# Optimization experiments

Hardware: AMD Instinct MI355X
Metric: run time of the kernel (lower is better)

The kernel has to match this reference:

```python
import jax, jax.numpy as jnp
import numpy as np

B, S, D = 4, 2048, 1024
NUM_HEADS = 16
KQ = D // NUM_HEADS  # 64


def setup_inputs() -> dict:
    key = jax.random.key(0)
    ks = jax.random.split(key, 4)
    # he_uniform fan_in = D: limit = sqrt(6/fan_in)
    lim = np.sqrt(6.0 / D).astype(np.float32)
    x = jax.random.normal(ks[0], (B, S, D), dtype=jnp.float32)
    Wq = jax.random.uniform(ks[1], (D, KQ), minval=-lim, maxval=lim, dtype=jnp.float32)
    Wk = jax.random.uniform(ks[2], (D, KQ), minval=-lim, maxval=lim, dtype=jnp.float32)
    Wv = jax.random.uniform(ks[3], (D, KQ), minval=-lim, maxval=lim, dtype=jnp.float32)
    Bq = jnp.zeros((S, KQ), dtype=jnp.float32)
    Bk = jnp.zeros((S, KQ), dtype=jnp.float32)
    Bv = jnp.zeros((S, KQ), dtype=jnp.float32)
    return {"x": x, "Wq": Wq, "Bq": Bq, "Wk": Wk, "Bk": Bk, "Wv": Wv, "Bv": Bv}


def reference(x, Wq, Bq, Wk, Bk, Wv, Bv):
    # Q/K/V: [B,S,KQ]; biases are per-position [S,KQ], broadcast over batch
    Q = jnp.einsum('bsd,dk->bsk', x, Wq) + Bq
    K = jnp.einsum('bsd,dk->bsk', x, Wk) + Bk
    V = jnp.einsum('bsd,dk->bsk', x, Wv) + Bv
    scale = 1.0 / jnp.sqrt(jnp.float32(KQ))
    scores = jnp.einsum('bqk,bsk->bqs', Q, K) * scale  # [B,S,S]
    attn = jax.nn.softmax(scores, axis=-1)
    return jnp.einsum('bqs,bsk->bqk', attn, V)  # [B,S,KQ]
```

## Files before the change

### kernel.cpp

```cpp
#include <hip/hip_runtime.h>
#include <stdint.h>

#define NBATCH 4
#define NS 2048
#define ND 1024
#define NK 64
#define QSCALE 0.18033688011112042f

typedef __attribute__((ext_vector_type(4))) float f32x4;
typedef __attribute__((ext_vector_type(16))) float f32x16;
typedef __attribute__((ext_vector_type(8))) short bf16x8;
typedef unsigned short u16;
typedef unsigned int u32;
typedef unsigned long long u64;

__device__ __forceinline__ u16 f2bf(float f) {
  union { float f; u32 u; } v; v.f = f;
  u32 u = v.u;
  u += 0x7FFFu + ((u >> 16) & 1u);
  return (u16)(u >> 16);
}

__device__ __forceinline__ u32 pk2(float lo, float hi) {
  u32 r;
  asm("v_cvt_pk_bf16_f32 %0, %1, %2" : "=v"(r) : "v"(lo), "v"(hi));
  return r;
}

__device__ __forceinline__ void gll16(const void* g, void* l) {
  __builtin_amdgcn_global_load_lds(
      (const __attribute__((address_space(1))) unsigned int*)g,
      (__attribute__((address_space(3))) unsigned int*)l, 16, 0, 0);
}

__global__ __launch_bounds__(256) void wtrans_kernel(
    const float* __restrict__ Wq, const float* __restrict__ Wk,
    const float* __restrict__ Wv, u16* __restrict__ Wt) {
  __shared__ float tile[64][65];
  int blk = blockIdx.x;
  int m = blk >> 4, dt = blk & 15;
  const float* W = (m == 0) ? Wq : (m == 1) ? Wk : Wv;
  int d0 = dt * 64;
  int t = threadIdx.x;
#pragma unroll
  for (int i = 0; i < 16; i++) {
    int idx = t + 256 * i;
    int dd = idx >> 6, c = idx & 63;
    tile[dd][c] = W[(d0 + dd) * 64 + c];
  }
  __syncthreads();
#pragma unroll
  for (int i = 0; i < 16; i++) {
    int idx = t + 256 * i;
    int c = idx >> 6, dd = idx & 63;
    Wt[(m * 64 + c) * 1024 + d0 + dd] = f2bf(tile[dd][c]);
  }
}

__global__ __launch_bounds__(512) void qkv_kernel(
    const float* __restrict__ x, const u16* __restrict__ Wt,
    const float* __restrict__ Bq, const float* __restrict__ Bk,
    const float* __restrict__ Bv, u16* __restrict__ Qf,
    u16* __restrict__ Kf, u16* __restrict__ Vf) {
  __shared__ __attribute__((aligned(16))) char lds[98304];
  char* ldsx = lds;
  char* ldsw = lds + 24576;

  int tid = threadIdx.x;
  int w = tid >> 6, lane = tid & 63;
  int g = lane >> 4, c = lane & 15;
  int rh = w & 1, cq = w >> 1;

  int xrow_l = 4 * w + (lane >> 4);
  long xrow_g = (long)blockIdx.x * 32 + xrow_l;
  int xs32 = ((lane >> 1) & 7) ^ (xrow_l & 7);
  const char* xg = (const char*)(x + xrow_g * ND) + xs32 * 32 + (lane & 1) * 16;

  int wr0 = 8 * w + (lane >> 3);
  const char* wg0 = (const char*)(Wt + (long)(wr0)       * ND) + (((lane & 7) ^ (wr0 & 7)) * 16);
  const char* wg1 = (const char*)(Wt + (long)(64 + wr0)  * ND) + (((lane & 7) ^ (wr0 & 7)) * 16);
  const char* wg2 = (const char*)(Wt + (long)(128 + wr0) * ND) + (((lane & 7) ^ (wr0 & 7)) * 16);
  int wd0 = (8 * w) * 128, wd1 = (64 + 8 * w) * 128, wd2 = (128 + 8 * w) * 128;

  int rowa = rh * 16 + c;
  int axor = rowa & 7;
  int aoff0 = rowa * 256 + ((g ^ axor) * 32);
  int aoff1 = rowa * 256 + (((4 + g) ^ axor) * 32);
  int boff[3][2];
#pragma unroll
  for (int tt = 0; tt < 3; tt++) {
    int col = cq * 48 + tt * 16 + c;
#pragma unroll
    for (int kk = 0; kk < 2; kk++)
      boff[tt][kk] = col * 128 + (((kk * 4 + g) ^ (col & 7)) * 16);
  }

  f32x4 acc[3];
#pragma unroll
  for (int tt = 0; tt < 3; tt++) acc[tt] = (f32x4){0.f, 0.f, 0.f, 0.f};

#define STAGE(BUF, T) do {                                            \
    gll16(xg + (long)(T) * 256, ldsx + (BUF) * 8192 + w * 1024);      \
    gll16(wg0 + (T) * 128, ldsw + (BUF) * 24576 + wd0);               \
    gll16(wg1 + (T) * 128, ldsw + (BUF) * 24576 + wd1);               \
    gll16(wg2 + (T) * 128, ldsw + (BUF) * 24576 + wd2);               \
  } while (0)

#define COMPUTE(B) do {                                               \
    const char* xb_ = ldsx + (B) * 8192;                              \
    const char* wb_ = ldsw + (B) * 24576;                             \
    f32x4 p0_ = *(const f32x4*)(xb_ + aoff0);                         \
    f32x4 p1_ = *(const f32x4*)(xb_ + aoff0 + 16);                    \
    f32x4 p2_ = *(const f32x4*)(xb_ + aoff1);                         \
    f32x4 p3_ = *(const f32x4*)(xb_ + aoff1 + 16);                    \
    union { bf16x8 v; u32 w[4]; } af0, af1;                           \
    af0.w[0] = pk2(p0_[0], p0_[1]); af0.w[1] = pk2(p0_[2], p0_[3]);   \
    af0.w[2] = pk2(p1_[0], p1_[1]); af0.w[3] = pk2(p1_[2], p1_[3]);   \
    af1.w[0] = pk2(p2_[0], p2_[1]); af1.w[1] = pk2(p2_[2], p2_[3]);   \
    af1.w[2] = pk2(p3_[0], p3_[1]); af1.w[3] = pk2(p3_[2], p3_[3]);   \
    _Pragma("unroll")                                                 \
    for (int tt = 0; tt < 3; tt++) {                                  \
      bf16x8 b0_ = *(const bf16x8*)(wb_ + boff[tt][0]);               \
      bf16x8 b1_ = *(const bf16x8*)(wb_ + boff[tt][1]);               \
      acc[tt] = __builtin_amdgcn_mfma_f32_16x16x32_bf16(af0.v, b0_, acc[tt], 0, 0, 0); \
      acc[tt] = __builtin_amdgcn_mfma_f32_16x16x32_bf16(af1.v, b1_, acc[tt], 0, 0, 0); \
    }                                                                 \
  } while (0)

  STAGE(0, 0);
  STAGE(1, 1);
#pragma unroll
  for (int t = 0; t < 16; t++) {
    if (t < 15) asm volatile("s_waitcnt vmcnt(4)" ::: "memory");
    else        asm volatile("s_waitcnt vmcnt(0)" ::: "memory");
    __builtin_amdgcn_s_barrier();
    __builtin_amdgcn_sched_barrier(0);
    if (t + 2 < 16) STAGE((t + 2) % 3, t + 2);
    __builtin_amdgcn_sched_barrier(0);
    COMPUTE(t % 3);
  }
#undef STAGE
#undef COMPUTE

  __syncthreads();
  u16* ep = (u16*)lds;
  int il = blockIdx.x & 63, bb = blockIdx.x >> 6;
#pragma unroll
  for (int tt = 0; tt < 3; tt++) {
    int colg = cq * 48 + tt * 16 + c;
    int mtx = colg >> 6;
    int col = colg & 63;
    const float* Bias = (mtx == 0) ? Bq : (mtx == 1) ? Bk : Bv;
#pragma unroll
    for (int j = 0; j < 4; j++) {
      int sl = rh * 16 + 4 * g + j;
      float v = acc[tt][j] + Bias[(il * 32 + sl) * NK + col];
      if (mtx == 0) v *= QSCALE;
      int chunk, off;
      if (mtx < 2) {
        chunk = mtx * 4 + (col >> 4);
        off = (sl + ((col >> 3) & 1) * 32) * 8 + (col & 7);
      } else {
        chunk = 8 + (col >> 5) * 2 + (sl >> 4);
        off = ((col & 31) + ((sl >> 3) & 1) * 32) * 8 + (sl & 7);
      }
      ep[chunk * 512 + off] = f2bf(v);
    }
  }
  __syncthreads();
  for (int t5 = tid; t5 < 768; t5 += 512) {
    int ch = t5 >> 6, pc = t5 & 63;
    bf16x8 val = *(const bf16x8*)(ep + ch * 512 + pc * 8);
    u16* dst;
    if (ch < 4)
      dst = Qf + (((long)bb * 64 + il) * 4 + ch) * 512 + pc * 8;
    else if (ch < 8)
      dst = Kf + (((long)bb * 64 + il) * 4 + (ch - 4)) * 512 + pc * 8;
    else {
      int half = (ch - 8) >> 1, iv = (ch - 8) & 1;
      dst = Vf + ((((long)bb * 2 + half) * 32 + (il >> 1)) * 4 + 2 * (il & 1) + iv) * 512 + pc * 8;
    }
    *(bf16x8*)dst = val;
  }
}

__device__ __forceinline__ bf16x8 pack8(float p0, float p1, float p2, float p3,
                                        float p4, float p5, float p6, float p7,
                                        int hi) {
  u32 A = pk2(p0, p1), B = pk2(p2, p3), C = pk2(p4, p5), D = pk2(p6, p7);
  u32 sA = (u32)__shfl_xor((int)A, 32);
  u32 sB = (u32)__shfl_xor((int)B, 32);
  u32 sC = (u32)__shfl_xor((int)C, 32);
  u32 sD = (u32)__shfl_xor((int)D, 32);
  union { u32 w[4]; bf16x8 v; } u;
  u.w[0] = hi ? sC : A;
  u.w[1] = hi ? sD : B;
  u.w[2] = hi ? C : sA;
  u.w[3] = hi ? D : sB;
  return u.v;
}

__global__ __launch_bounds__(512) __attribute__((amdgpu_waves_per_eu(2, 2)))
void attn_kernel(
    const u16* __restrict__ Qf, const u16* __restrict__ Kf,
    const u16* __restrict__ Vf, float* __restrict__ out) {
  __shared__ float Ol[8][32][64];
  __shared__ float Ll[8][32];
  int w = threadIdx.x >> 6, lane = threadIdx.x & 63;
  int q = lane & 31, hi = lane >> 5;
  int bid = blockIdx.x;
  int b = (bid & 7) >> 1;
  int qt = ((bid >> 3) << 1) | (bid & 1);
  long qglob = (long)b * NS + qt * 32;

  bf16x8 qf[4];
  {
    const u16* qp = Qf + ((long)b * 64 + qt) * 2048 + lane * 8;
#pragma unroll
    for (int kk = 0; kk < 4; kk++) qf[kk] = *(const bf16x8*)(qp + kk * 512);
  }
  const u16* kcp = Kf + ((long)b * 64 + w * 8) * 2048 + lane * 8;
  const u16* vcp0 = Vf + ((long)b * 64 + w * 4) * 2048 + lane * 8;
  const u16* vcp1 = Vf + ((long)(b * 2 + 1) * 32 + w * 4) * 2048 + lane * 8;

  f32x16 o0, o1;
#pragma unroll
  for (int r = 0; r < 16; r++) { o0[r] = 0.f; o1[r] = 0.f; }
  float lacc[4] = {0.f, 0.f, 0.f, 0.f};

  bf16x8 kA0[4], kA1[4], kB0[4], kB1[4];
#pragma unroll
  for (int kk = 0; kk < 4; kk++) {
    kA0[kk] = *(const bf16x8*)(kcp + kk * 512);
    kA1[kk] = *(const bf16x8*)(kcp + 2048 + kk * 512);
  }

#define ATTN_STEP(T, KC0, KC1, KN0, KN1)                                      \
  do {                                                                        \
    int t_ = (T);                                                             \
    bf16x8 vf0[4], vf1[4];                                                    \
    _Pragma("unroll") for (int i = 0; i < 4; i++) {                           \
      vf0[i] = *(const bf16x8*)(vcp0 + t_ * 2048 + i * 512);                  \
      vf1[i] = *(const bf16x8*)(vcp1 + t_ * 2048 + i * 512);                  \
    }                                                                         \
    if (t_ + 1 < 4) {                                                         \
      const u16* kn_ = kcp + (long)(t_ + 1) * 4096;                           \
      _Pragma("unroll") for (int i = 0; i < 4; i++) {                         \
        KN0[i] = *(const bf16x8*)(kn_ + i * 512);                             \
        KN1[i] = *(const bf16x8*)(kn_ + 2048 + i * 512);                      \
      }                                                                       \
    }                                                                         \
    __builtin_amdgcn_sched_barrier(0);                                        \
    f32x16 s0, s1;                                                            \
    _Pragma("unroll") for (int r = 0; r < 16; r++) { s0[r] = 0.f; s1[r] = 0.f; } \
    _Pragma("unroll") for (int i = 0; i < 4; i++)                             \
      s0 = __builtin_amdgcn_mfma_f32_32x32x16_bf16(KC0[i], qf[i], s0, 0, 0, 0); \
    _Pragma("unroll") for (int i = 0; i < 4; i++)                             \
      s1 = __builtin_amdgcn_mfma_f32_32x32x16_bf16(KC1[i], qf[i], s1, 0, 0, 0); \
    _Pragma("unroll") for (int r = 0; r < 16; r++) {                          \
      s0[r] = exp2f(s0[r]); s1[r] = exp2f(s1[r]);                             \
      lacc[r & 3] += s0[r] + s1[r];                                           \
    }                                                                         \
    bf16x8 pa[4];                                                             \
    pa[0] = pack8(s0[0], s0[1], s0[2], s0[3], s0[4], s0[5], s0[6], s0[7], hi);   \
    pa[1] = pack8(s0[8], s0[9], s0[10], s0[11], s0[12], s0[13], s0[14], s0[15], hi); \
    pa[2] = pack8(s1[0], s1[1], s1[2], s1[3], s1[4], s1[5], s1[6], s1[7], hi);   \
    pa[3] = pack8(s1[8], s1[9], s1[10], s1[11], s1[12], s1[13], s1[14], s1[15], hi); \
    _Pragma("unroll") for (int i = 0; i < 4; i++) {                           \
      o0 = __builtin_amdgcn_mfma_f32_32x32x16_bf16(pa[i], vf0[i], o0, 0, 0, 0); \
      o1 = __builtin_amdgcn_mfma_f32_32x32x16_bf16(pa[i], vf1[i], o1, 0, 0, 0); \
    }                                                                         \
  } while (0)

  ATTN_STEP(0, kA0, kA1, kB0, kB1);
  ATTN_STEP(1, kB0, kB1, kA0, kA1);
  ATTN_STEP(2, kA0, kA1, kB0, kB1);
  ATTN_STEP(3, kB0, kB1, kA0, kA1);
#undef ATTN_STEP

  float lt = (lacc[0] + lacc[1]) + (lacc[2] + lacc[3]);
  lt += __shfl_xor(lt, 32);

#pragma unroll
  for (int r = 0; r < 16; r++) {
    int qq = (r & 3) + 8 * (r >> 2) + 4 * hi;
    Ol[w][qq][q]      = o0[r];
    Ol[w][qq][q + 32] = o1[r];
  }
  if (hi == 0) Ll[w][q] = lt;
  __syncthreads();

#pragma unroll
  for (int rr = 4; rr >= 1; rr >>= 1) {
    if (w < rr) {
#pragma unroll
      for (int i = 0; i < 8; i++) {
        int idx = lane + i * 64;
        f32x4* dst = (f32x4*)&Ol[w][idx >> 4][(idx & 15) * 4];
        const f32x4* src = (const f32x4*)&Ol[w + rr][idx >> 4][(idx & 15) * 4];
        *dst += *src;
      }
      if (lane < 32) Ll[w][lane] += Ll[w + rr][lane];
    }
    __syncthreads();
  }

  {
    int idx = threadIdx.x;
    int row = idx >> 4, c4 = (idx & 15) * 4;
    float inv = 1.0f / Ll[0][row];
    f32x4 v = *(const f32x4*)&Ol[0][row][c4];
    f32x4 r;
#pragma unroll
    for (int i = 0; i < 4; i++) r[i] = v[i] * inv;
    *(f32x4*)&out[(qglob + row) * NK + c4] = r;
  }
}

extern "C" void kernel_launch(void* const* d_in, const int* in_sizes, int n_in,
                              void* d_out, int out_size, void* d_ws, size_t ws_size,
                              hipStream_t stream) {
  const float* x  = (const float*)d_in[0];
  const float* Wq = (const float*)d_in[1];
  const float* Bq = (const float*)d_in[2];
  const float* Wk = (const float*)d_in[3];
  const float* Bk = (const float*)d_in[4];
  const float* Wv = (const float*)d_in[5];
  const float* Bv = (const float*)d_in[6];
  float* out = (float*)d_out;

  char* ws = (char*)d_ws;
  u16* Wt = (u16*)ws;
  u16* Qf = (u16*)(ws + 393216);
  u16* Kf = (u16*)(ws + 1441792);
  u16* Vf = (u16*)(ws + 2490368);

  wtrans_kernel<<<dim3(48), dim3(256), 0, stream>>>(Wq, Wk, Wv, Wt);
  qkv_kernel<<<dim3(256), dim3(512), 0, stream>>>(x, Wt, Bq, Bk, Bv, Qf, Kf, Vf);
  attn_kernel<<<dim3(256), dim3(512), 0, stream>>>(Qf, Kf, Vf, out);
}
```

Before: 31.69 us.

## Load pre-swizzled weight fragments straight to registers in QKV projection

The weight-transpose kernel now writes bf16 weights in the exact MFMA B-fragment order, so the QKV kernel loads B operands directly from global memory into registers instead of staging them through LDS. LDS use drops to a double-buffered x tile, and the pipeline goes from triple to double buffering with a full vmcnt wait and block barrier each iteration. The kernel is also pinned to two waves per EU. This removes LDS traffic and capacity pressure for weights, but every wave now refetches weight fragments from global or L2 memory and there is less load/compute overlap.

New measurement: 36.62 us. 15.5% more time.

```diff
diff --git a/kernel.cpp b/kernel.cpp
--- a/kernel.cpp
+++ b/kernel.cpp
@@ -35,7 +35,7 @@
 
 __global__ __launch_bounds__(256) void wtrans_kernel(
     const float* __restrict__ Wq, const float* __restrict__ Wk,
-    const float* __restrict__ Wv, u16* __restrict__ Wt) {
+    const float* __restrict__ Wv, u16* __restrict__ Wtf) {
   __shared__ float tile[64][65];
   int blk = blockIdx.x;
   int m = blk >> 4, dt = blk & 15;
@@ -49,22 +49,28 @@
     tile[dd][c] = W[(d0 + dd) * 64 + c];
   }
   __syncthreads();
-#pragma unroll
-  for (int i = 0; i < 16; i++) {
-    int idx = t + 256 * i;
-    int c = idx >> 6, dd = idx & 63;
-    Wt[(m * 64 + c) * 1024 + d0 + dd] = f2bf(tile[dd][c]);
-  }
-}
-
-__global__ __launch_bounds__(512) void qkv_kernel(
-    const float* __restrict__ x, const u16* __restrict__ Wt,
+  int j = t >> 6, lane = t & 63;
+  int gidx = m * 4 + j;
+  int cq = gidx / 3, tt = gidx % 3;
+  int cc = j * 16 + (lane & 15);
+  int kb = (lane >> 4) * 8;
+#pragma unroll
+  for (int kk = 0; kk < 2; kk++) {
+    int chunk = ((dt * 4 + cq) * 3 + tt) * 2 + kk;
+    union { u16 u[8]; bf16x8 v; } pk;
+#pragma unroll
+    for (int e = 0; e < 8; e++) pk.u[e] = f2bf(tile[kk * 32 + kb + e][cc]);
+    *(bf16x8*)&Wtf[chunk * 512 + lane * 8] = pk.v;
+  }
+}
+
+__global__ __launch_bounds__(512) __attribute__((amdgpu_waves_per_eu(2, 2)))
+void qkv_kernel(
+    const float* __restrict__ x, const u16* __restrict__ Wtf,
     const float* __restrict__ Bq, const float* __restrict__ Bk,
     const float* __restrict__ Bv, u16* __restrict__ Qf,
     u16* __restrict__ Kf, u16* __restrict__ Vf) {
-  __shared__ __attribute__((aligned(16))) char lds[98304];
-  char* ldsx = lds;
-  char* ldsw = lds + 24576;
+  __shared__ __attribute__((aligned(16))) char lds[16384];
 
   int tid = threadIdx.x;
   int w = tid >> 6, lane = tid & 63;
@@ -76,39 +82,30 @@
   int xs32 = ((lane >> 1) & 7) ^ (xrow_l & 7);
   const char* xg = (const char*)(x + xrow_g * ND) + xs32 * 32 + (lane & 1) * 16;
 
-  int wr0 = 8 * w + (lane >> 3);
-  const char* wg0 = (const char*)(Wt + (long)(wr0)       * ND) + (((lane & 7) ^ (wr0 & 7)) * 16);
-  const char* wg1 = (const char*)(Wt + (long)(64 + wr0)  * ND) + (((lane & 7) ^ (wr0 & 7)) * 16);
-  const char* wg2 = (const char*)(Wt + (long)(128 + wr0) * ND) + (((lane & 7) ^ (wr0 & 7)) * 16);
-  int wd0 = (8 * w) * 128, wd1 = (64 + 8 * w) * 128, wd2 = (128 + 8 * w) * 128;
-
   int rowa = rh * 16 + c;
   int axor = rowa & 7;
   int aoff0 = rowa * 256 + ((g ^ axor) * 32);
   int aoff1 = rowa * 256 + (((4 + g) ^ axor) * 32);
-  int boff[3][2];
-#pragma unroll
-  for (int tt = 0; tt < 3; tt++) {
-    int col = cq * 48 + tt * 16 + c;
-#pragma unroll
-    for (int kk = 0; kk < 2; kk++)
-      boff[tt][kk] = col * 128 + (((kk * 4 + g) ^ (col & 7)) * 16);
-  }
 
   f32x4 acc[3];
 #pragma unroll
   for (int tt = 0; tt < 3; tt++) acc[tt] = (f32x4){0.f, 0.f, 0.f, 0.f};
 
-#define STAGE(BUF, T) do {                                            \
-    gll16(xg + (long)(T) * 256, ldsx + (BUF) * 8192 + w * 1024);      \
-    gll16(wg0 + (T) * 128, ldsw + (BUF) * 24576 + wd0);               \
-    gll16(wg1 + (T) * 128, ldsw + (BUF) * 24576 + wd1);               \
-    gll16(wg2 + (T) * 128, ldsw + (BUF) * 24576 + wd2);               \
+  bf16x8 breg[2][6];
+  const u16* wfl = Wtf + lane * 8;
+
+#define LOADB(BUF, T) do {                                            \
+    const u16* wb_ = wfl + (long)(((T) * 4 + cq) * 6) * 512;          \
+    breg[BUF][0] = *(const bf16x8*)(wb_);                             \
+    breg[BUF][1] = *(const bf16x8*)(wb_ + 512);                       \
+    breg[BUF][2] = *(const bf16x8*)(wb_ + 1024);                      \
+    breg[BUF][3] = *(const bf16x8*)(wb_ + 1536);                      \
+    breg[BUF][4] = *(const bf16x8*)(wb_ + 2048);                      \
+    breg[BUF][5] = *(const bf16x8*)(wb_ + 2560);                      \
   } while (0)
 
 #define COMPUTE(B) do {                                               \
-    const char* xb_ = ldsx + (B) * 8192;                              \
-    const char* wb_ = ldsw + (B) * 24576;                             \
+    const char* xb_ = lds + (B) * 8192;                               \
     f32x4 p0_ = *(const f32x4*)(xb_ + aoff0);                         \
     f32x4 p1_ = *(const f32x4*)(xb_ + aoff0 + 16);                    \
     f32x4 p2_ = *(const f32x4*)(xb_ + aoff1);                         \
@@ -120,29 +117,29 @@
     af1.w[2] = pk2(p3_[0], p3_[1]); af1.w[3] = pk2(p3_[2], p3_[3]);   \
     _Pragma("unroll")                                                 \
     for (int tt = 0; tt < 3; tt++) {                                  \
-      bf16x8 b0_ = *(const bf16x8*)(wb_ + boff[tt][0]);               \
-      bf16x8 b1_ = *(const bf16x8*)(wb_ + boff[tt][1]);               \
-      acc[tt] = __builtin_amdgcn_mfma_f32_16x16x32_bf16(af0.v, b0_, acc[tt], 0, 0, 0); \
-      acc[tt] = __builtin_amdgcn_mfma_f32_16x16x32_bf16(af1.v, b1_, acc[tt], 0, 0, 0); \
+      acc[tt] = __builtin_amdgcn_mfma_f32_16x16x32_bf16(af0.v, breg[B][tt * 2],     acc[tt], 0, 0, 0); \
+      acc[tt] = __builtin_amdgcn_mfma_f32_16x16x32_bf16(af1.v, breg[B][tt * 2 + 1], acc[tt], 0, 0, 0); \
     }                                                                 \
   } while (0)
 
-  STAGE(0, 0);
-  STAGE(1, 1);
+  gll16(xg, lds + w * 1024);
+  LOADB(0, 0);
+  asm volatile("s_waitcnt vmcnt(0)" ::: "memory");
+  __syncthreads();
+
 #pragma unroll
   for (int t = 0; t < 16; t++) {
-    if (t < 15) asm volatile("s_waitcnt vmcnt(4)" ::: "memory");
-    else        asm volatile("s_waitcnt vmcnt(0)" ::: "memory");
-    __builtin_amdgcn_s_barrier();
-    __builtin_amdgcn_sched_barrier(0);
-    if (t + 2 < 16) STAGE((t + 2) % 3, t + 2);
-    __builtin_amdgcn_sched_barrier(0);
-    COMPUTE(t % 3);
-  }
-#undef STAGE
+    if (t < 15) {
+      gll16(xg + (long)(t + 1) * 256, lds + ((t + 1) & 1) * 8192 + w * 1024);
+      LOADB((t + 1) & 1, t + 1);
+    }
+    COMPUTE(t & 1);
+    asm volatile("s_waitcnt vmcnt(0)" ::: "memory");
+    __syncthreads();
+  }
+#undef LOADB
 #undef COMPUTE
 
-  __syncthreads();
   u16* ep = (u16*)lds;
   int il = blockIdx.x & 63, bb = blockIdx.x >> 6;
 #pragma unroll
@@ -330,12 +327,12 @@
   float* out = (float*)d_out;
 
   char* ws = (char*)d_ws;
-  u16* Wt = (u16*)ws;
+  u16* Wtf = (u16*)ws;
   u16* Qf = (u16*)(ws + 393216);
   u16* Kf = (u16*)(ws + 1441792);
   u16* Vf = (u16*)(ws + 2490368);
 
-  wtrans_kernel<<<dim3(48), dim3(256), 0, stream>>>(Wq, Wk, Wv, Wt);
-  qkv_kernel<<<dim3(256), dim3(512), 0, stream>>>(x, Wt, Bq, Bk, Bv, Qf, Kf, Vf);
+  wtrans_kernel<<<dim3(48), dim3(256), 0, stream>>>(Wq, Wk, Wv, Wtf);
+  qkv_kernel<<<dim3(256), dim3(512), 0, stream>>>(x, Wtf, Bq, Bk, Bv, Qf, Kf, Vf);
   attn_kernel<<<dim3(256), dim3(512), 0, stream>>>(Qf, Kf, Vf, out);
 }
```

## Split attention KV range across two blocks and add combine kernel

Applied to the files above, without the earlier changes.

The attention kernel now runs 512 blocks of 4 waves instead of 256 blocks of 8 waves. Each block covers half of the key/value sequence and writes unnormalized partial outputs and row sums to workspace. A new combine kernel adds the two partials and normalizes. The goal is more, smaller blocks to improve CU occupancy and scheduling, and a shorter in-block reduction. The cost is an extra kernel launch plus a global round trip for the partial results.

Result: slower. 34.67 us (+9.4%).

```diff
diff --git a/kernel.cpp b/kernel.cpp
--- a/kernel.cpp
+++ b/kernel.cpp
@@ -200,17 +200,19 @@
   return u.v;
 }
 
-__global__ __launch_bounds__(512) __attribute__((amdgpu_waves_per_eu(2, 2)))
+__global__ __launch_bounds__(256) __attribute__((amdgpu_waves_per_eu(2, 2)))
 void attn_kernel(
     const u16* __restrict__ Qf, const u16* __restrict__ Kf,
-    const u16* __restrict__ Vf, float* __restrict__ out) {
-  __shared__ float Ol[8][32][64];
-  __shared__ float Ll[8][32];
+    const u16* __restrict__ Vf, float* __restrict__ Opart,
+    float* __restrict__ lpart) {
+  __shared__ float Ol[4][32][64];
+  __shared__ float Ll[4][32];
   int w = threadIdx.x >> 6, lane = threadIdx.x & 63;
   int q = lane & 31, hi = lane >> 5;
   int bid = blockIdx.x;
   int b = (bid & 7) >> 1;
-  int qt = ((bid >> 3) << 1) | (bid & 1);
+  int half = (bid >> 3) & 1;
+  int qt = ((bid >> 4) << 1) | (bid & 1);
   long qglob = (long)b * NS + qt * 32;
 
   bf16x8 qf[4];
@@ -219,9 +221,9 @@
 #pragma unroll
     for (int kk = 0; kk < 4; kk++) qf[kk] = *(const bf16x8*)(qp + kk * 512);
   }
-  const u16* kcp = Kf + ((long)b * 64 + w * 8) * 2048 + lane * 8;
-  const u16* vcp0 = Vf + ((long)b * 64 + w * 4) * 2048 + lane * 8;
-  const u16* vcp1 = Vf + ((long)(b * 2 + 1) * 32 + w * 4) * 2048 + lane * 8;
+  const u16* kcp = Kf + ((long)b * 64 + half * 32 + w * 8) * 2048 + lane * 8;
+  const u16* vcp0 = Vf + ((long)(b * 2) * 32 + half * 16 + w * 4) * 2048 + lane * 8;
+  const u16* vcp1 = Vf + ((long)(b * 2 + 1) * 32 + half * 16 + w * 4) * 2048 + lane * 8;
 
   f32x16 o0, o1;
 #pragma unroll
@@ -291,7 +293,7 @@
   __syncthreads();
 
 #pragma unroll
-  for (int rr = 4; rr >= 1; rr >>= 1) {
+  for (int rr = 2; rr >= 1; rr >>= 1) {
     if (w < rr) {
 #pragma unroll
       for (int i = 0; i < 8; i++) {
@@ -305,16 +307,34 @@
     __syncthreads();
   }
 
-  {
-    int idx = threadIdx.x;
+  long ob = (long)half * (NBATCH * NS * NK);
+#pragma unroll
+  for (int ii = 0; ii < 2; ii++) {
+    int idx = threadIdx.x + ii * 256;
     int row = idx >> 4, c4 = (idx & 15) * 4;
-    float inv = 1.0f / Ll[0][row];
     f32x4 v = *(const f32x4*)&Ol[0][row][c4];
-    f32x4 r;
-#pragma unroll
-    for (int i = 0; i < 4; i++) r[i] = v[i] * inv;
-    *(f32x4*)&out[(qglob + row) * NK + c4] = r;
-  }
+    *(f32x4*)&Opart[ob + (qglob + row) * NK + c4] = v;
+  }
+  if (threadIdx.x < 32)
+    lpart[half * (NBATCH * NS) + qglob + threadIdx.x] = Ll[0][threadIdx.x];
+}
+
+__global__ __launch_bounds__(256) void combine_kernel(
+    const float* __restrict__ Opart, const float* __restrict__ lpart,
+    float* __restrict__ out, int nsplit) {
+  int gid = blockIdx.x * 256 + threadIdx.x;
+  int rw = gid >> 4, c4 = (gid & 15) * 4;
+  f32x4 a = (f32x4){0.f, 0.f, 0.f, 0.f};
+  float l = 0.f;
+  for (int sp = 0; sp < nsplit; sp++) {
+    a += *(const f32x4*)(Opart + (long)sp * (NBATCH * NS * NK) + (long)rw * NK + c4);
+    l += lpart[sp * (NBATCH * NS) + rw];
+  }
+  float inv = 1.0f / l;
+  f32x4 r;
+#pragma unroll
+  for (int i = 0; i < 4; i++) r[i] = a[i] * inv;
+  *(f32x4*)(out + (long)rw * NK + c4) = r;
 }
 
 extern "C" void kernel_launch(void* const* d_in, const int* in_sizes, int n_in,
@@ -334,8 +354,11 @@
   u16* Qf = (u16*)(ws + 393216);
   u16* Kf = (u16*)(ws + 1441792);
   u16* Vf = (u16*)(ws + 2490368);
+  float* lpart = (float*)(ws + 3538944);
+  float* Opart = (float*)(ws + 3801088);
 
   wtrans_kernel<<<dim3(48), dim3(256), 0, stream>>>(Wq, Wk, Wv, Wt);
   qkv_kernel<<<dim3(256), dim3(512), 0, stream>>>(x, Wt, Bq, Bk, Bv, Qf, Kf, Vf);
-  attn_kernel<<<dim3(256), dim3(512), 0, stream>>>(Qf, Kf, Vf, out);
-}
+  attn_kernel<<<dim3(512), dim3(256), 0, stream>>>(Qf, Kf, Vf, Opart, lpart);
+  combine_kernel<<<dim3(512), dim3(256), 0, stream>>>(Opart, lpart, out, 2);
+}
```
